# Performance work log

Measured on AMD Instinct MI355X. Metric: run time of the kernel, lower is better.

The kernel has to match this reference:

```python
import jax, jax.numpy as jnp
import numpy as np

B, S, D, H = 4, 2048, 2048, 16
HD = D // H  # 128
ROPE_THETA = 10000.0


def apply_rope(x, pos, theta=ROPE_THETA):
    # x: [b, h, s, d], pos: [s] int. Interleaved-pair RoPE.
    d = x.shape[-1]
    inv_freq = theta ** (-jnp.arange(0, d, 2, dtype=jnp.float32) / d)  # [d/2]
    ang = pos.astype(jnp.float32)[:, None] * inv_freq[None, :]         # [s, d/2]
    cos, sin = jnp.cos(ang), jnp.sin(ang)
    x1, x2 = x[..., ::2], x[..., 1::2]                                  # [b,h,s,d/2]
    r1 = x1 * cos - x2 * sin
    r2 = x1 * sin + x2 * cos
    return jnp.stack([r1, r2], axis=-1).reshape(x.shape).astype(x.dtype)


def setup_inputs() -> dict:
    key = jax.random.key(0)
    kx, kq, kk, kv, ko = jax.random.split(key, 5)
    w_scale = 0.02
    return {
        "x": jax.random.normal(kx, (B, S, D), dtype=jnp.float32),
        "wq": jax.random.normal(kq, (D, D), dtype=jnp.float32) * w_scale,
        "wk": jax.random.normal(kk, (D, D), dtype=jnp.float32) * w_scale,
        "wv": jax.random.normal(kv, (D, D), dtype=jnp.float32) * w_scale,
        "wo": jax.random.normal(ko, (D, D), dtype=jnp.float32) * w_scale,
        "token_positions": jnp.arange(S, dtype=jnp.int32),
    }


def reference(x, wq, wk, wv, wo, token_positions):
    b, s, d = x.shape
    # QKV projections: weight layout is [d_out, d_in] (torch nn.Parameter convention)
    Q = jnp.einsum("bsd,kd->bsk", x, wq).reshape(b, s, H, HD).transpose(0, 2, 1, 3)
    K = jnp.einsum("bsd,kd->bsk", x, wk).reshape(b, s, H, HD).transpose(0, 2, 1, 3)
    V = jnp.einsum("bsd,kd->bsk", x, wv).reshape(b, s, H, HD).transpose(0, 2, 1, 3)
    Q = apply_rope(Q, token_positions)
    K = apply_rope(K, token_positions)
    # naive causal attention: full [b,h,s,s] score matrix
    scores = jnp.einsum("bhqd,bhkd->bhqk", Q, K) / jnp.sqrt(jnp.float32(HD))
    causal = jnp.tril(jnp.ones((s, s), dtype=bool))
    neg_inf = jnp.finfo(scores.dtype).min
    scores = jnp.where(causal[None, None], scores, neg_inf)
    probs = jax.nn.softmax(scores, axis=-1)
    O = jnp.einsum("bhqk,bhkd->bhqd", probs, V)
    O = O.transpose(0, 2, 1, 3).reshape(b, s, H * HD)
    return jnp.einsum("bsv,dv->bsd", O, wo)
```

## Files before the change

kernel.cpp:

```cpp
#include <hip/hip_runtime.h>
#include <cstdint>

typedef _Float16 f16;
typedef __attribute__((ext_vector_type(8))) _Float16 f16x8;
typedef __attribute__((ext_vector_type(4))) float f32x4;

constexpr int Bc  = 4;
constexpr int Sc  = 2048;
constexpr int Dc  = 2048;
constexpr int Hc  = 16;
constexpr int HDc = 128;

__global__ void cast_all_kernel(const float* __restrict__ x,  const float* __restrict__ wq,
                                const float* __restrict__ wk, const float* __restrict__ wv,
                                const float* __restrict__ wo,
                                f16* __restrict__ xh,  f16* __restrict__ wqh,
                                f16* __restrict__ wkh, f16* __restrict__ wvh,
                                f16* __restrict__ woh)
{
    long bid = blockIdx.x;
    const float* src; f16* dst; long off;
    if (bid < 8192)       { src = x;  dst = xh;  off = bid * 2048; }
    else {
        int r = (int)((bid - 8192) >> 11);
        off = ((bid - 8192) & 2047) * 2048;
        switch (r) {
            case 0:  src = wq; dst = wqh; break;
            case 1:  src = wk; dst = wkh; break;
            case 2:  src = wv; dst = wvh; break;
            default: src = wo; dst = woh; break;
        }
    }
    long i = off + (long)threadIdx.x * 8;
    float4 a = *(const float4*)(src + i);
    float4 b = *(const float4*)(src + i + 4);
    f16x8 o = { (f16)a.x, (f16)a.y, (f16)a.z, (f16)a.w,
                (f16)b.x, (f16)b.y, (f16)b.z, (f16)b.w };
    *(f16x8*)(dst + i) = o;
}

__device__ __forceinline__ void async_cp16(const f16* g, f16* l)
{
    __builtin_amdgcn_global_load_lds(
        (__attribute__((address_space(1))) void*)(g),
        (__attribute__((address_space(3))) void*)(l), 16, 0, 0);
}

template<typename OUT_T>
__global__ __launch_bounds__(512, 2) void gemm_bt8(
    const f16* __restrict__ A, const f16* __restrict__ W,
    OUT_T* __restrict__ C, int M, int N, int K)
{
    __shared__ alignas(16) f16 As[4][8192];
    __shared__ alignas(16) f16 Bs[4][8192];

    const int tid  = threadIdx.x;
    const int wave = tid >> 6, lane = tid & 63;
    const int l16  = lane & 15, quad = lane >> 4;
    const int wm   = wave >> 2, wn = wave & 3;

    const int nwg = (int)gridDim.x;
    int bid = (int)blockIdx.x;
    int wg  = ((nwg & 7) == 0) ? ((bid & 7) * (nwg >> 3) + (bid >> 3)) : bid;
    const int ntile = N >> 8;
    const int mt = wg / ntile, nt = wg % ntile;
    const int m0 = mt << 8, n0 = nt << 8;

    const int  prow = tid >> 2;
    const int  lch  = (((tid & 3) ^ ((prow >> 1) & 3)) << 3);
    const f16* Asrc = A + (long)(m0 + prow) * K + lch;
    const f16* Bsrc = W + (long)(n0 + prow) * K + lch;
    const long rsk  = (long)K << 7;
    const int  dst0 = wave << 9;

    const int nkt = K >> 5;

    auto stA = [&](int kt) {
        const f16* g = Asrc + ((long)kt << 5);
        int s = kt & 3;
        async_cp16(g,       &As[s][dst0]);
        async_cp16(g + rsk, &As[s][4096 + dst0]);
    };
    auto stB = [&](int kt) {
        const f16* g = Bsrc + ((long)kt << 5);
        int s = kt & 3;
        async_cp16(g,       &Bs[s][dst0]);
        async_cp16(g + rsk, &Bs[s][4096 + dst0]);
    };

    const int coff = ((quad ^ ((l16 >> 1) & 3)) << 3);
    const int arow = wm * 128 + l16;
    const int brow = wn * 64  + l16;

    f32x4 acc[8][4];
#pragma unroll
    for (int i = 0; i < 8; i++)
#pragma unroll
        for (int j = 0; j < 4; j++) acc[i][j] = (f32x4){0.f, 0.f, 0.f, 0.f};

    stA(0); stB(0);
    if (nkt > 1) {
        stA(1); stB(1);
        asm volatile("s_waitcnt vmcnt(4)");
    } else {
        asm volatile("s_waitcnt vmcnt(0)");
    }
    __builtin_amdgcn_s_barrier();
    __builtin_amdgcn_sched_barrier(0);

    for (int kt = 0; kt < nkt; ++kt) {
        const int s = kt & 3;
        const f16* as = &As[s][(long)arow * 32 + coff];
        const f16* bs = &Bs[s][(long)brow * 32 + coff];

        f16x8 bfr[4], afr[4];
#pragma unroll
        for (int j = 0; j < 4; ++j) bfr[j] = *(const f16x8*)(bs + j * 512);
#pragma unroll
        for (int i = 0; i < 4; ++i) afr[i] = *(const f16x8*)(as + i * 512);
        if (kt + 2 < nkt) stA(kt + 2);
        __builtin_amdgcn_s_barrier();
        asm volatile("s_waitcnt lgkmcnt(0)");
        __builtin_amdgcn_sched_barrier(0);
        __builtin_amdgcn_s_setprio(1);
#pragma unroll
        for (int i = 0; i < 4; ++i)
#pragma unroll
            for (int j = 0; j < 4; ++j)
                acc[i][j] = __builtin_amdgcn_mfma_f32_16x16x32_f16(afr[i], bfr[j], acc[i][j], 0, 0, 0);
        __builtin_amdgcn_s_setprio(0);
        __builtin_amdgcn_s_barrier();

#pragma unroll
        for (int i = 0; i < 4; ++i) afr[i] = *(const f16x8*)(as + (i + 4) * 512);
        if (kt + 2 < nkt) stB(kt + 2);
        __builtin_amdgcn_s_barrier();
        asm volatile("s_waitcnt lgkmcnt(0)");
        __builtin_amdgcn_sched_barrier(0);
        __builtin_amdgcn_s_setprio(1);
#pragma unroll
        for (int i = 0; i < 4; ++i)
#pragma unroll
            for (int j = 0; j < 4; ++j)
                acc[i + 4][j] = __builtin_amdgcn_mfma_f32_16x16x32_f16(afr[i], bfr[j], acc[i + 4][j], 0, 0, 0);
        __builtin_amdgcn_s_setprio(0);

        if (kt + 2 < nkt) asm volatile("s_waitcnt vmcnt(4)");
        else              asm volatile("s_waitcnt vmcnt(0)");
        __builtin_amdgcn_s_barrier();
        __builtin_amdgcn_sched_barrier(0);
    }

#pragma unroll
    for (int i = 0; i < 8; ++i) {
        int row = m0 + wm * 128 + i * 16 + quad * 4;
#pragma unroll
        for (int j = 0; j < 4; ++j) {
            int col = n0 + wn * 64 + j * 16 + l16;
#pragma unroll
            for (int r = 0; r < 4; ++r)
                C[(long)(row + r) * N + col] = (OUT_T)acc[i][j][r];
        }
    }
}

__global__ void rope_kernel(f16* __restrict__ Q, f16* __restrict__ K,
                            const int* __restrict__ pos, long npairs)
{
    long t = (long)blockIdx.x * blockDim.x + threadIdx.x;
    if (t >= 2 * npairs) return;
    f16* P = Q;
    long p = t;
    if (p >= npairs) { P = K; p -= npairs; }
    int  i    = (int)(p & 63);
    long rest = p >> 6;
    int  h    = (int)(rest & (Hc - 1));
    long row  = rest >> 4;
    int  s    = (int)(row & (Sc - 1));

    float inv = expf(-(float)i * (9.210340371976184f / 64.0f));
    float ang = (float)pos[s] * inv;
    float sn, cs;
    sincosf(ang, &sn, &cs);

    long idx = row * Dc + (long)h * HDc + 2 * i;
    unsigned int u = *(const unsigned int*)(P + idx);
    float x1 = (float)((const f16*)&u)[0];
    float x2 = (float)((const f16*)&u)[1];
    f16 o[2] = { (f16)(x1 * cs - x2 * sn), (f16)(x1 * sn + x2 * cs) };
    *(unsigned int*)(P + idx) = *(const unsigned int*)o;
}


__device__ __forceinline__ int swz(int row, int col, int ldshift) {
    return (row << ldshift) + (((((col >> 3) ^ ((row >> 1) & 7)) << 3) | (col & 7)));
}

__global__ __launch_bounds__(256, 2) void attn_kernel(
    const f16* __restrict__ Q, const f16* __restrict__ Kg,
    const f16* __restrict__ Vg, f16* __restrict__ O)
{
    __shared__ alignas(16) f16 Kt[2][64 * 128];
    __shared__ alignas(16) f16 Vt[128 * 64];
    __shared__ alignas(16) f16 Pl[128 * 64];

    const int tid  = threadIdx.x;
    const int wave = tid >> 6, lane = tid & 63;
    const int l16  = lane & 15, quad = lane >> 4;

    const int L  = (int)blockIdx.x;
    const int bh = (L & 7) + 8 * (L >> 7);
    const int qi = 15 - ((L >> 3) & 15);
    const int b  = bh >> 4, h = bh & 15;
    const long base = (long)b * Sc * Dc + (long)h * HDc;
    const float cexp = 0.12751742366f;

    long koff[4];
    f16* kdst[4];
#pragma unroll
    for (int j = 0; j < 4; j++) {
        int row_l = j * 16 + wave * 4 + (lane >> 4);
        int chg   = (lane & 15) ^ ((row_l >> 1) & 7);
        koff[j]   = base + (long)row_l * Dc + chg * 8;
        kdst[j]   = (f16*)&Kt[0][(j * 16 + wave * 4) * 128];
    }
    const int vd0 = lane * 2;

    f16x8 ones;
#pragma unroll
    for (int i = 0; i < 8; i++) ones[i] = (f16)1.0f;

    unsigned int vreg[2][8];
    auto load_v = [&](int k0) {
#pragma unroll
        for (int j = 0; j < 2; j++) {
            int kk0 = wave * 8 + j * 32;
#pragma unroll
            for (int i2 = 0; i2 < 8; i2++)
                vreg[j][i2] = *(const unsigned int*)&Vg[base + (long)(k0 + kk0 + i2) * Dc + vd0];
        }
    };
    auto load_k_async = [&](int k0, int buf) {
        long bufoff = (long)buf * (64 * 128);
#pragma unroll
        for (int j = 0; j < 4; j++)
            async_cp16(Kg + koff[j] + (long)k0 * Dc, kdst[j] + bufoff);
    };

    const int q0  = qi * 128;
    const int nkt = 2 * qi + 2;
    const int rlo = q0 + wave * 32;

    f16x8 qf[2][4];
#pragma unroll
    for (int im = 0; im < 2; im++)
#pragma unroll
        for (int kk = 0; kk < 4; kk++)
            qf[im][kk] = *(const f16x8*)&Q[base + (long)(q0 + wave * 32 + im * 16 + l16) * Dc
                                           + kk * 32 + quad * 8];

    f32x4 oacc[2][8];
    f32x4 lacc[2];
#pragma unroll
    for (int im = 0; im < 2; im++) {
        lacc[im] = (f32x4){0.f, 0.f, 0.f, 0.f};
#pragma unroll
        for (int nt = 0; nt < 8; nt++) oacc[im][nt] = (f32x4){0.f, 0.f, 0.f, 0.f};
    }

    load_k_async(0, 0);
    load_v(0);
    for (int kt = 0; kt < nkt; kt++) {
        const int k0  = kt * 64;
        const int buf = kt & 1;
        __syncthreads();
#pragma unroll
        for (int j = 0; j < 2; j++) {
            int kk0 = wave * 8 + j * 32;
            f16x8 lo, hi;
#pragma unroll
            for (int i2 = 0; i2 < 8; i2++) {
                lo[i2] = ((const f16*)&vreg[j][i2])[0];
                hi[i2] = ((const f16*)&vreg[j][i2])[1];
            }
            *(f16x8*)&Vt[swz(vd0,     kk0, 6)] = lo;
            *(f16x8*)&Vt[swz(vd0 + 1, kk0, 6)] = hi;
        }
        __syncthreads();
        if (kt + 1 < nkt) {
            load_k_async(k0 + 64, buf ^ 1);
            load_v(k0 + 64);
        }

        if (k0 <= rlo + 31) {
            f32x4 sf[2][4];
#pragma unroll
            for (int im = 0; im < 2; im++)
#pragma unroll
                for (int in = 0; in < 4; in++) sf[im][in] = (f32x4){0.f, 0.f, 0.f, 0.f};
#pragma unroll
            for (int kk = 0; kk < 4; kk++) {
                f16x8 bf[4];
#pragma unroll
                for (int in = 0; in < 4; in++)
                    bf[in] = *(const f16x8*)&Kt[buf][swz(in * 16 + l16, kk * 32 + quad * 8, 7)];
#pragma unroll
                for (int im = 0; im < 2; im++)
#pragma unroll
                    for (int in = 0; in < 4; in++)
                        sf[im][in] = __builtin_amdgcn_mfma_f32_16x16x32_f16(qf[im][kk], bf[in], sf[im][in], 0, 0, 0);
            }

#pragma unroll
            for (int im = 0; im < 2; im++) {
                const int rbase = rlo + im * 16;
                const bool need_mask = (k0 + 63 > rbase);
#pragma unroll
                for (int in = 0; in < 4; in++) {
#pragma unroll
                    for (int r = 0; r < 4; r++) {
                        float p = __builtin_amdgcn_exp2f(sf[im][in][r] * cexp);
                        if (need_mask) {
                            int kc  = k0 + in * 16 + l16;
                            int row = rbase + quad * 4 + r;
                            p = (kc <= row) ? p : 0.f;
                        }
                        Pl[swz(wave * 32 + im * 16 + quad * 4 + r, in * 16 + l16, 6)] = (f16)p;
                    }
                }
            }

#pragma unroll
            for (int kk = 0; kk < 2; kk++) {
                f16x8 pf[2];
#pragma unroll
                for (int im = 0; im < 2; im++)
                    pf[im] = *(const f16x8*)&Pl[swz(wave * 32 + im * 16 + l16, kk * 32 + quad * 8, 6)];
#pragma unroll
                for (int im = 0; im < 2; im++)
                    lacc[im] = __builtin_amdgcn_mfma_f32_16x16x32_f16(pf[im], ones, lacc[im], 0, 0, 0);
#pragma unroll
                for (int nt = 0; nt < 8; nt++) {
                    f16x8 vf = *(const f16x8*)&Vt[swz(nt * 16 + l16, kk * 32 + quad * 8, 6)];
#pragma unroll
                    for (int im = 0; im < 2; im++)
                        oacc[im][nt] = __builtin_amdgcn_mfma_f32_16x16x32_f16(pf[im], vf, oacc[im][nt], 0, 0, 0);
                }
            }
        }
    }

#pragma unroll
    for (int im = 0; im < 2; im++) {
        int qrow = q0 + wave * 32 + im * 16 + quad * 4;
#pragma unroll
        for (int r = 0; r < 4; r++) {
            float inv = 1.0f / lacc[im][r];
#pragma unroll
            for (int nt = 0; nt < 8; nt++)
                O[base + (long)(qrow + r) * Dc + nt * 16 + l16] = (f16)(oacc[im][nt][r] * inv);
        }
    }
}

extern "C" void kernel_launch(void* const* d_in, const int* in_sizes, int n_in,
                              void* d_out, int out_size, void* d_ws, size_t ws_size,
                              hipStream_t stream)
{
    const float* x  = (const float*)d_in[0];
    const float* wq = (const float*)d_in[1];
    const float* wk = (const float*)d_in[2];
    const float* wv = (const float*)d_in[3];
    const float* wo = (const float*)d_in[4];
    const int*  pos = (const int*)d_in[5];
    float* out = (float*)d_out;

    const long E = (long)Bc * Sc * Dc;
    const long W = (long)Dc * Dc;
    f16* ws  = (f16*)d_ws;
    f16* xh  = ws;
    f16* wqh = ws + E;
    f16* wkh = wqh + W;
    f16* wvh = wkh + W;
    f16* woh = wvh + W;
    f16* Qh  = woh + W;
    f16* Kh  = Qh + E;
    f16* Vh  = Kh + E;
    f16* Oh  = xh;

    cast_all_kernel<<<dim3(16384), 256, 0, stream>>>(x, wq, wk, wv, wo,
                                                     xh, wqh, wkh, wvh, woh);

    dim3 gg((Bc * Sc / 256) * (Dc / 256));
    gemm_bt8<f16><<<gg, 512, 0, stream>>>(xh, wqh, Qh, Bc * Sc, Dc, Dc);
    gemm_bt8<f16><<<gg, 512, 0, stream>>>(xh, wkh, Kh, Bc * Sc, Dc, Dc);
    gemm_bt8<f16><<<gg, 512, 0, stream>>>(xh, wvh, Vh, Bc * Sc, Dc, Dc);

    long npairs = (long)Bc * Sc * Hc * (HDc / 2);
    rope_kernel<<<dim3(2 * npairs / 256), 256, 0, stream>>>(Qh, Kh, pos, npairs);

    attn_kernel<<<dim3(1024), 256, 0, stream>>>(Qh, Kh, Vh, Oh);

    gemm_bt8<float><<<gg, 512, 0, stream>>>(Oh, woh, out, Bc * Sc, Dc, Dc);
}
```

Baseline: 640.3 us.

## Single-buffer K tile in attention for 3 blocks/CU; drop GEMM mid-loop barriers

The attention kernel drops the double-buffered K tile in shared memory to a single buffer and raises launch bounds from 2 to 3 blocks per CU, to lift occupancy. An extra __syncthreads is added after QK^T so the next K/V prefetch can overwrite the buffer, which delays the prefetch and shortens its overlap with compute. In the GEMM, two intra-iteration s_barriers are removed, a separate register array holds the second A fragment half, and the waitcnt asm gains memory clobbers. Whether the 4-stage GEMM ring is safe without those barriers depends on the lgkmcnt/vmcnt ordering.

```diff
diff --git a/kernel.cpp b/kernel.cpp
--- a/kernel.cpp
+++ b/kernel.cpp
@@ -101,9 +101,9 @@
     stA(0); stB(0);
     if (nkt > 1) {
         stA(1); stB(1);
-        asm volatile("s_waitcnt vmcnt(4)");
+        asm volatile("s_waitcnt vmcnt(4)" ::: "memory");
     } else {
-        asm volatile("s_waitcnt vmcnt(0)");
+        asm volatile("s_waitcnt vmcnt(0)" ::: "memory");
     }
     __builtin_amdgcn_s_barrier();
     __builtin_amdgcn_sched_barrier(0);
@@ -119,8 +119,7 @@
 #pragma unroll
         for (int i = 0; i < 4; ++i) afr[i] = *(const f16x8*)(as + i * 512);
         if (kt + 2 < nkt) stA(kt + 2);
-        __builtin_amdgcn_s_barrier();
-        asm volatile("s_waitcnt lgkmcnt(0)");
+        asm volatile("s_waitcnt lgkmcnt(0)" ::: "memory");
         __builtin_amdgcn_sched_barrier(0);
         __builtin_amdgcn_s_setprio(1);
 #pragma unroll
@@ -129,24 +128,23 @@
             for (int j = 0; j < 4; ++j)
                 acc[i][j] = __builtin_amdgcn_mfma_f32_16x16x32_f16(afr[i], bfr[j], acc[i][j], 0, 0, 0);
         __builtin_amdgcn_s_setprio(0);
-        __builtin_amdgcn_s_barrier();
-
-#pragma unroll
-        for (int i = 0; i < 4; ++i) afr[i] = *(const f16x8*)(as + (i + 4) * 512);
+
+        f16x8 afr2[4];
+#pragma unroll
+        for (int i = 0; i < 4; ++i) afr2[i] = *(const f16x8*)(as + (i + 4) * 512);
         if (kt + 2 < nkt) stB(kt + 2);
-        __builtin_amdgcn_s_barrier();
-        asm volatile("s_waitcnt lgkmcnt(0)");
+        asm volatile("s_waitcnt lgkmcnt(0)" ::: "memory");
         __builtin_amdgcn_sched_barrier(0);
         __builtin_amdgcn_s_setprio(1);
 #pragma unroll
         for (int i = 0; i < 4; ++i)
 #pragma unroll
             for (int j = 0; j < 4; ++j)
-                acc[i + 4][j] = __builtin_amdgcn_mfma_f32_16x16x32_f16(afr[i], bfr[j], acc[i + 4][j], 0, 0, 0);
+                acc[i + 4][j] = __builtin_amdgcn_mfma_f32_16x16x32_f16(afr2[i], bfr[j], acc[i + 4][j], 0, 0, 0);
         __builtin_amdgcn_s_setprio(0);
 
-        if (kt + 2 < nkt) asm volatile("s_waitcnt vmcnt(4)");
-        else              asm volatile("s_waitcnt vmcnt(0)");
+        if (kt + 2 < nkt) asm volatile("s_waitcnt vmcnt(4)" ::: "memory");
+        else              asm volatile("s_waitcnt vmcnt(0)" ::: "memory");
         __builtin_amdgcn_s_barrier();
         __builtin_amdgcn_sched_barrier(0);
     }
@@ -191,16 +189,15 @@
     *(unsigned int*)(P + idx) = *(const unsigned int*)o;
 }
 
-
 __device__ __forceinline__ int swz(int row, int col, int ldshift) {
     return (row << ldshift) + (((((col >> 3) ^ ((row >> 1) & 7)) << 3) | (col & 7)));
 }
 
-__global__ __launch_bounds__(256, 2) void attn_kernel(
+__global__ __launch_bounds__(256, 3) void attn_kernel(
     const f16* __restrict__ Q, const f16* __restrict__ Kg,
     const f16* __restrict__ Vg, f16* __restrict__ O)
 {
-    __shared__ alignas(16) f16 Kt[2][64 * 128];
+    __shared__ alignas(16) f16 Kt[64 * 128];
     __shared__ alignas(16) f16 Vt[128 * 64];
     __shared__ alignas(16) f16 Pl[128 * 64];
 
@@ -222,7 +219,7 @@
         int row_l = j * 16 + wave * 4 + (lane >> 4);
         int chg   = (lane & 15) ^ ((row_l >> 1) & 7);
         koff[j]   = base + (long)row_l * Dc + chg * 8;
-        kdst[j]   = (f16*)&Kt[0][(j * 16 + wave * 4) * 128];
+        kdst[j]   = (f16*)&Kt[(j * 16 + wave * 4) * 128];
     }
     const int vd0 = lane * 2;
 
@@ -240,11 +237,10 @@
                 vreg[j][i2] = *(const unsigned int*)&Vg[base + (long)(k0 + kk0 + i2) * Dc + vd0];
         }
     };
-    auto load_k_async = [&](int k0, int buf) {
-        long bufoff = (long)buf * (64 * 128);
+    auto load_k_async = [&](int k0) {
 #pragma unroll
         for (int j = 0; j < 4; j++)
-            async_cp16(Kg + koff[j] + (long)k0 * Dc, kdst[j] + bufoff);
+            async_cp16(Kg + koff[j] + (long)k0 * Dc, kdst[j]);
     };
 
     const int q0  = qi * 128;
@@ -268,11 +264,10 @@
         for (int nt = 0; nt < 8; nt++) oacc[im][nt] = (f32x4){0.f, 0.f, 0.f, 0.f};
     }
 
-    load_k_async(0, 0);
+    load_k_async(0);
     load_v(0);
     for (int kt = 0; kt < nkt; kt++) {
-        const int k0  = kt * 64;
-        const int buf = kt & 1;
+        const int k0 = kt * 64;
         __syncthreads();
 #pragma unroll
         for (int j = 0; j < 2; j++) {
@@ -287,13 +282,10 @@
             *(f16x8*)&Vt[swz(vd0 + 1, kk0, 6)] = hi;
         }
         __syncthreads();
-        if (kt + 1 < nkt) {
-            load_k_async(k0 + 64, buf ^ 1);
-            load_v(k0 + 64);
-        }
-
-        if (k0 <= rlo + 31) {
-            f32x4 sf[2][4];
+
+        const bool compute = (k0 <= rlo + 31);
+        f32x4 sf[2][4];
+        if (compute) {
 #pragma unroll
             for (int im = 0; im < 2; im++)
 #pragma unroll
@@ -303,14 +295,22 @@
                 f16x8 bf[4];
 #pragma unroll
                 for (int in = 0; in < 4; in++)
-                    bf[in] = *(const f16x8*)&Kt[buf][swz(in * 16 + l16, kk * 32 + quad * 8, 7)];
+                    bf[in] = *(const f16x8*)&Kt[swz(in * 16 + l16, kk * 32 + quad * 8, 7)];
 #pragma unroll
                 for (int im = 0; im < 2; im++)
 #pragma unroll
                     for (int in = 0; in < 4; in++)
                         sf[im][in] = __builtin_amdgcn_mfma_f32_16x16x32_f16(qf[im][kk], bf[in], sf[im][in], 0, 0, 0);
             }
-
+        }
+        __syncthreads();
+
+        if (kt + 1 < nkt) {
+            load_k_async(k0 + 64);
+            load_v(k0 + 64);
+        }
+
+        if (compute) {
 #pragma unroll
             for (int im = 0; im < 2; im++) {
                 const int rbase = rlo + im * 16;
```

Result: slower. 1.034 ms (+61.4%).
